# Kernel optimization log

Measured on AMD Instinct MI355X. Metric: run time of the kernel, lower is better.

Reference implementation:

```python
import jax, jax.numpy as jnp
import numpy as np
from jax import lax

B, N_ENT, D_ENT = 64, 512, 256
C_SCAT, C_MAP, W = 32, 18, 64
N_RES = 4


def conv2d(x, w, stride, pad):
    return lax.conv_general_dilated(x, w, (stride, stride), [(pad, pad), (pad, pad)],
                                    dimension_numbers=('NCHW', 'OIHW', 'NCHW'))


def batchnorm(x, g, b, eps=1e-5):
    # training-mode BN (batch statistics), matching nn.BatchNorm2d default train()
    mu = x.mean((0, 2, 3), keepdims=True)
    var = x.var((0, 2, 3), keepdims=True)
    return g[None, :, None, None] * (x - mu) * lax.rsqrt(var + eps) + b[None, :, None, None]


def setup_inputs() -> dict:
    key = jax.random.key(0)
    ks = jax.random.split(key, 24)
    s = 0.05
    inp = {
        'x': jax.random.uniform(ks[0], (B, C_MAP, W, W), jnp.float32),
        'entity_embeddings': jax.random.normal(ks[1], (B, N_ENT, D_ENT), jnp.float32),
        'entity_x_y': jax.random.randint(ks[2], (B, N_ENT, 16), 0, 2, jnp.int32),
        'conv1_w': jax.random.normal(ks[3], (C_SCAT, D_ENT), jnp.float32) * s,
        'project_w': jax.random.normal(ks[4], (32, C_SCAT + C_MAP, 1, 1), jnp.float32) * s,
        'project_b': jnp.zeros((32,), jnp.float32),
        'ds1_w': jax.random.normal(ks[5], (64, 32, 4, 4), jnp.float32) * s,
        'ds1_b': jnp.zeros((64,), jnp.float32),
        'ds2_w': jax.random.normal(ks[6], (128, 64, 4, 4), jnp.float32) * s,
        'ds2_b': jnp.zeros((128,), jnp.float32),
        'ds3_w': jax.random.normal(ks[7], (128, 128, 4, 4), jnp.float32) * s,
        'ds3_b': jnp.zeros((128,), jnp.float32),
        'res_conv1_w': jax.random.normal(ks[8], (N_RES, 128, 128, 3, 3), jnp.float32) * s,
        'res_bn1_g': jnp.ones((N_RES, 128), jnp.float32),
        'res_bn1_b': jnp.zeros((N_RES, 128), jnp.float32),
        'res_conv2_w': jax.random.normal(ks[9], (N_RES, 128, 128, 3, 3), jnp.float32) * s,
        'res_bn2_g': jnp.ones((N_RES, 128), jnp.float32),
        'res_bn2_b': jnp.zeros((N_RES, 128), jnp.float32),
        'fc_w': jax.random.normal(ks[10], (256, 8 * 8 * 128), jnp.float32) * s,
        'fc_b': jnp.zeros((256,), jnp.float32),
    }
    return inp


def _scatter(entity_embeddings, entity_x_y, conv1_w):
    # reduced = relu(Conv1d(256->32, k=1)) on entity dim
    reduced = jax.nn.relu(jnp.einsum('bnd,cd->bnc', entity_embeddings, conv1_w))  # [B,N,32]
    bits = entity_x_y
    pow2 = (2 ** jnp.arange(7, -1, -1)).astype(jnp.int32)
    xv = (bits[..., :8] * pow2).sum(-1) // 4   # [B,N] in 0..63
    yv = (bits[..., 8:] * pow2).sum(-1) // 4
    valid = (bits[..., 0] != -1000000000)
    reduced = reduced * valid[..., None].astype(reduced.dtype)
    b_idx = jnp.arange(entity_embeddings.shape[0], dtype=jnp.int32)[:, None]
    flat = (b_idx * (W * W) + yv * W + xv).reshape(-1)
    scat = jax.ops.segment_sum(reduced.reshape(-1, C_SCAT), flat, num_segments=entity_embeddings.shape[0] * W * W)
    return scat.reshape(-1, W, W, C_SCAT).transpose(0, 3, 1, 2)  # [B,32,W,W]


def reference(x, entity_embeddings, entity_x_y, conv1_w, project_w, project_b,
              ds1_w, ds1_b, ds2_w, ds2_b, ds3_w, ds3_b,
              res_conv1_w, res_bn1_g, res_bn1_b, res_conv2_w, res_bn2_g, res_bn2_b,
              fc_w, fc_b):
    scatter_map = _scatter(entity_embeddings, entity_x_y, conv1_w)
    h = jnp.concatenate([scatter_map, x], axis=1)  # [B,50,64,64]
    h = jax.nn.relu(conv2d(h, project_w, 1, 0) + project_b[None, :, None, None])
    h = jax.nn.relu(conv2d(h, ds1_w, 2, 1) + ds1_b[None, :, None, None])   # [B,64,32,32]
    h = jax.nn.relu(conv2d(h, ds2_w, 2, 1) + ds2_b[None, :, None, None])   # [B,128,16,16]
    h = jax.nn.relu(conv2d(h, ds3_w, 2, 1) + ds3_b[None, :, None, None])   # [B,128,8,8]
    map_skip = h
    for i in range(N_RES):
        identity = h
        o = batchnorm(conv2d(h, res_conv1_w[i], 1, 1), res_bn1_g[i], res_bn1_b[i])
        o = jax.nn.relu(o)
        o = batchnorm(conv2d(o, res_conv2_w[i], 1, 1), res_bn2_g[i], res_bn2_b[i])
        h = jax.nn.relu(o + identity)
        map_skip = map_skip + h
    flat = h.reshape(h.shape[0], -1)
    embedded_spatial = jax.nn.relu(flat @ fc_w.T + fc_b)
    return (map_skip, embedded_spatial)
```

## Files before the change

### kernel.cpp

```cpp
#include <hip/hip_runtime.h>
#include <hip/hip_bf16.h>

typedef __attribute__((ext_vector_type(8))) short bf16x8;
typedef __attribute__((ext_vector_type(4))) short bf16x4;
typedef __attribute__((ext_vector_type(4))) float f32x4;

__device__ __forceinline__ short f2bs(float v) {
  __hip_bfloat16 h = __float2bfloat16(v);
  return *reinterpret_cast<short*>(&h);
}

__global__ __launch_bounds__(256) void k_wall(
    const float* __restrict__ rc1w, const float* __restrict__ rc2w,
    const float* __restrict__ d1w, const float* __restrict__ d2w,
    const float* __restrict__ d3w, const float* __restrict__ fcw,
    const float* __restrict__ c1w, const float* __restrict__ pw,
    short* __restrict__ wTr1, short* __restrict__ wTr2, short* __restrict__ wTds1,
    short* __restrict__ wTds2, short* __restrict__ wTds3, short* __restrict__ wfcbf,
    short* __restrict__ wsc, short* __restrict__ wproj,
    float* __restrict__ scatz, float* __restrict__ statsz) {
  __shared__ float ld[128 * 65];
  const int bx = blockIdx.x;
  const int tid = threadIdx.x;
  if (bx < 4608) {
    const float* src = (bx < 2304) ? rc1w : rc2w;
    short* dst = (bx < 2304) ? wTr1 : wTr2;
    const int i = (bx % 2304) * 256 + tid;
    if (i < 589824) {
      const int layer = i / 147456;
      const int rem = i % 147456;
      const int tap = rem / 16384;
      const int r2 = rem & 16383;
      const int co = r2 >> 7, ci = r2 & 127;
      dst[i] = f2bs(src[(((size_t)layer * 16384 + co * 128 + ci) * 9) + tap]);
    }
  } else if (bx < 6272) {
    int CIN, n, base;
    const float* src;
    short* dst;
    if (bx < 4736) { CIN = 32; n = 32768; base = 4608; src = d1w; dst = wTds1; }
    else if (bx < 5248) { CIN = 64; n = 131072; base = 4736; src = d2w; dst = wTds2; }
    else { CIN = 128; n = 262144; base = 5248; src = d3w; dst = wTds3; }
    const int i = (bx - base) * 256 + tid;
    if (i < n) {
      const int COCI = n / 16;
      const int tap = i / COCI;
      const int rem = i % COCI;
      dst[i] = f2bs(src[(size_t)rem * 16 + tap]);
    }
  } else if (bx < 6528) {
    const int j = bx - 6272;
    const float* sp = fcw + (size_t)j * 8192;
    for (int i = tid; i < 8192; i += 256) {
      const int co = i >> 6, pix = i & 63;
      ld[co * 65 + pix] = sp[i];
    }
    __syncthreads();
    short* dp = wfcbf + (size_t)j * 8192;
    for (int i = tid; i < 8192; i += 256) {
      const int pix = i >> 7, co = i & 127;
      dp[i] = f2bs(ld[co * 65 + pix]);
    }
  } else if (bx < 6560) {
    const int i = (bx - 6528) * 256 + tid;
    if (i < 8192) wsc[i] = f2bs(c1w[i]);
  } else if (bx < 6568) {
    const int i = (bx - 6560) * 256 + tid;
    if (i < 2048) {
      const int co = i >> 6, k = i & 63;
      wproj[i] = (k < 50) ? f2bs(pw[co * 50 + k]) : (short)0;
    }
  } else if (bx < 7080) {
    float4* dst = (float4*)(scatz + (size_t)(bx - 6568) * 16384);
    const float4 z = {0.f, 0.f, 0.f, 0.f};
    for (int t = tid; t < 4096; t += 256) dst[t] = z;
  } else {
    for (int i = tid; i < 2064; i += 256) statsz[i] = 0.f;
  }
}

__global__ __launch_bounds__(256) void k_scatmfma(const float* __restrict__ emb,
                                                  const int* __restrict__ xy,
                                                  const short* __restrict__ wsc,
                                                  float* __restrict__ scat_pm) {
  constexpr int CIP = 264;
  __shared__ short abf[64 * CIP];
  __shared__ int flat[64];
  const int tid = threadIdx.x;
  const int e0 = blockIdx.x * 64;
  const float4* eg = (const float4*)(emb + (size_t)e0 * 256);
  for (int i = tid; i < 4096; i += 256) {
    const int e = i >> 6, k4 = i & 63;
    const float4 v = eg[(size_t)e * 64 + k4];
    bf16x4 o;
    o[0] = f2bs(v.x); o[1] = f2bs(v.y); o[2] = f2bs(v.z); o[3] = f2bs(v.w);
    *(bf16x4*)(&abf[e * CIP + k4 * 4]) = o;
  }
  if (tid < 64) {
    const int* bp = xy + (size_t)(e0 + tid) * 16;
    int xv = 0, yv = 0;
#pragma unroll
    for (int j = 0; j < 8; ++j) xv = (xv << 1) | bp[j];
#pragma unroll
    for (int j = 8; j < 16; ++j) yv = (yv << 1) | bp[j];
    flat[tid] = (bp[0] != -1000000000)
                    ? (((e0 + tid) >> 9) * 4096 + ((yv >> 2) << 6) + (xv >> 2))
                    : -1;
  }
  __syncthreads();
  const int wq = __builtin_amdgcn_readfirstlane(tid >> 6);
  const int lane = tid & 63;
  const int l15 = lane & 15, quad = lane >> 4;
  f32x4 acc[2];
  acc[0] = (f32x4){0.f, 0.f, 0.f, 0.f};
  acc[1] = (f32x4){0.f, 0.f, 0.f, 0.f};
  const short* arow = &abf[(wq * 16 + l15) * CIP + quad * 8];
  const short* w0 = wsc + (size_t)l15 * 256 + quad * 8;
  const short* w1 = wsc + (size_t)(16 + l15) * 256 + quad * 8;
#pragma unroll
  for (int kk = 0; kk < 8; ++kk) {
    bf16x8 a = *(const bf16x8*)(arow + kk * 32);
    acc[0] = __builtin_amdgcn_mfma_f32_16x16x32_bf16(a, *(const bf16x8*)(w0 + kk * 32), acc[0], 0, 0, 0);
    acc[1] = __builtin_amdgcn_mfma_f32_16x16x32_bf16(a, *(const bf16x8*)(w1 + kk * 32), acc[1], 0, 0, 0);
  }
#pragma unroll
  for (int nt = 0; nt < 2; ++nt)
#pragma unroll
    for (int r = 0; r < 4; ++r) {
      const int e = wq * 16 + quad * 4 + r;
      const float v = acc[nt][r];
      const int f = flat[e];
      if (f >= 0 && v > 0.f)
        atomicAdd(&scat_pm[(size_t)f * 32 + nt * 16 + l15], v);
    }
}

__global__ __launch_bounds__(256) void k_projmfma(const float* __restrict__ scat_pm,
                                                  const float* __restrict__ xin,
                                                  const short* __restrict__ wproj,
                                                  const float* __restrict__ pb,
                                                  short* __restrict__ h0pm) {
  constexpr int PK = 72;
  __shared__ short abf[128 * PK];
  const int tid = threadIdx.x;
  const int b = blockIdx.x >> 5;
  const int yx0 = (blockIdx.x & 31) << 7;
  const float4* sg = (const float4*)(scat_pm + ((size_t)(b * 4096 + yx0)) * 32);
  for (int i = tid; i < 1024; i += 256) {
    const int p = i >> 3, c4 = i & 7;
    const float4 v = sg[(size_t)p * 8 + c4];
    bf16x4 o;
    o[0] = f2bs(v.x); o[1] = f2bs(v.y); o[2] = f2bs(v.z); o[3] = f2bs(v.w);
    *(bf16x4*)(&abf[p * PK + c4 * 4]) = o;
  }
  for (int i = tid; i < 2304; i += 256) {
    const int run = i >> 7, p = i & 127;
    abf[p * PK + 32 + run] = f2bs(xin[(size_t)(b * 18 + run) * 4096 + yx0 + p]);
  }
  for (int i = tid; i < 2048; i += 256) {
    const int p = i >> 4, k = 50 + (i & 15);
    abf[p * PK + k] = 0;
  }
  __syncthreads();
  const int wq = __builtin_amdgcn_readfirstlane(tid >> 6);
  const int lane = tid & 63;
  const int l15 = lane & 15, quad = lane >> 4;
  f32x4 acc[2][2];
#pragma unroll
  for (int t = 0; t < 2; ++t)
#pragma unroll
    for (int n = 0; n < 2; ++n) acc[t][n] = (f32x4){0.f, 0.f, 0.f, 0.f};
  const short* wb0 = wproj + (size_t)l15 * 64 + quad * 8;
  const short* wb1 = wproj + (size_t)(16 + l15) * 64 + quad * 8;
#pragma unroll
  for (int kk = 0; kk < 2; ++kk) {
    const bf16x8 b0 = *(const bf16x8*)(wb0 + kk * 32);
    const bf16x8 b1 = *(const bf16x8*)(wb1 + kk * 32);
#pragma unroll
    for (int t = 0; t < 2; ++t) {
      const int pix = (wq * 2 + t) * 16 + l15;
      bf16x8 a = *(const bf16x8*)(&abf[pix * PK + quad * 8 + kk * 32]);
      acc[t][0] = __builtin_amdgcn_mfma_f32_16x16x32_bf16(a, b0, acc[t][0], 0, 0, 0);
      acc[t][1] = __builtin_amdgcn_mfma_f32_16x16x32_bf16(a, b1, acc[t][1], 0, 0, 0);
    }
  }
#pragma unroll
  for (int t = 0; t < 2; ++t)
#pragma unroll
    for (int n = 0; n < 2; ++n) {
      const int co = n * 16 + l15;
      const float bv = pb[co];
#pragma unroll
      for (int r = 0; r < 4; ++r) {
        const int pix = (wq * 2 + t) * 16 + quad * 4 + r;
        float v = acc[t][n][r] + bv;
        v = v > 0.f ? v : 0.f;
        h0pm[((size_t)(b * 4096 + yx0 + pix)) * 32 + co] = f2bs(v);
      }
    }
}

template <int CIN, int COUT, int HIN, int ROWSO, int COSPLIT, int MT, int NT, int OUTMODE>
__global__ __launch_bounds__(256) void k_ds2(const short* __restrict__ inpm,
                                             const short* __restrict__ wT,
                                             const float* __restrict__ bias,
                                             short* __restrict__ outbf,
                                             float* __restrict__ outf,
                                             float* __restrict__ msf) {
  constexpr int HOUT = HIN / 2;
  constexpr int ROWS = 2 * ROWSO + 2;
  constexpr int COLS = HIN + 2;
  constexpr int CHUNKS = CIN / 8;
  constexpr int KK = CIN / 32;
  constexpr int CIPAD = CIN + 8;
  constexpr int NHO = HOUT / ROWSO;
  __shared__ short lin[ROWS * COLS * CIPAD];
  const int tid = threadIdx.x;
  int bx = blockIdx.x;
  const int co_blk = (COSPLIT > 1) ? (bx % COSPLIT) : 0;
  if (COSPLIT > 1) bx /= COSPLIT;
  const int hoblk = bx % NHO;
  const int b = bx / NHO;
  for (int i = tid; i < ROWS * COLS * CHUNKS; i += 256) {
    const int ch = i % CHUNKS;
    const int pixv = i / CHUNKS;
    const int r = pixv / COLS, c = pixv % COLS;
    const int hi = 2 * ROWSO * hoblk - 1 + r;
    const int wc = c - 1;
    bf16x8 v = (bf16x8)(short)0;
    if (hi >= 0 && hi < HIN && wc >= 0 && wc < HIN)
      v = *(const bf16x8*)(inpm + ((size_t)(b * HIN + hi) * HIN + wc) * CIN + ch * 8);
    *(bf16x8*)(&lin[(r * COLS + c) * CIPAD + ch * 8]) = v;
  }
  __syncthreads();
  const int wq = __builtin_amdgcn_readfirstlane(tid >> 6);
  const int lane = tid & 63;
  const int l15 = lane & 15, quad = lane >> 4;
  const int mtile = (MT > 1) ? (wq % MT) : 0;
  const int cogrp = wq / MT;
  const int cobase = co_blk * (COUT / COSPLIT) + cogrp * (NT * 16);
  const int p = mtile * 16 + l15;
  const int dr = p / HOUT;
  const int col = p % HOUT;
  f32x4 acc[NT];
#pragma unroll
  for (int n = 0; n < NT; ++n) acc[n] = (f32x4){0.f, 0.f, 0.f, 0.f};
  const short* wrow = wT + (size_t)(cobase + l15) * CIN + quad * 8;
  for (int ky = 0; ky < 4; ++ky) {
    for (int kx = 0; kx < 4; ++kx) {
      const short* arow = &lin[((2 * dr + ky) * COLS + 2 * col + kx) * CIPAD + quad * 8];
      const short* wt = wrow + (size_t)(ky * 4 + kx) * COUT * CIN;
#pragma unroll
      for (int kk = 0; kk < KK; ++kk) {
        bf16x8 a = *(const bf16x8*)(arow + kk * 32);
#pragma unroll
        for (int n = 0; n < NT; ++n) {
          bf16x8 bf = *(const bf16x8*)(wt + n * 16 * CIN + kk * 32);
          acc[n] = __builtin_amdgcn_mfma_f32_16x16x32_bf16(a, bf, acc[n], 0, 0, 0);
        }
      }
    }
  }
#pragma unroll
  for (int n = 0; n < NT; ++n) {
    const int co = cobase + n * 16 + l15;
    const float bv = bias[co];
#pragma unroll
    for (int r = 0; r < 4; ++r) {
      const int pp = mtile * 16 + quad * 4 + r;
      const int dr2 = pp / HOUT;
      const int c2 = pp % HOUT;
      const int ho = hoblk * ROWSO + dr2;
      float v = acc[n][r] + bv;
      v = v > 0.f ? v : 0.f;
      const size_t o = ((size_t)b * HOUT * HOUT + ho * HOUT + c2) * COUT + co;
      outbf[o] = f2bs(v);
      if (OUTMODE == 1) {
        outf[o] = v;
        msf[o] = v;
      }
    }
  }
}

template <int BNIN>
__global__ __launch_bounds__(256) void k_resmfma(const short* __restrict__ hbfin,
                                                 const float* __restrict__ fin,
                                                 const float* __restrict__ statsIn,
                                                 const float* __restrict__ gIn,
                                                 const float* __restrict__ bIn,
                                                 const short* __restrict__ wT,
                                                 float* __restrict__ outpm,
                                                 float* __restrict__ statsOut) {
  constexpr int CIPAD = 136;
  __shared__ short lin[100 * CIPAD];
  __shared__ float bnsc[128], bnsh[128];
  const int tid = threadIdx.x;
  const int b = blockIdx.x >> 3;
  const int cobase = (blockIdx.x & 7) << 4;
  if (BNIN == 1) {
    if (tid < 128) {
      const float mu = statsIn[tid] * (1.f / 4096.f);
      const float var = statsIn[128 + tid] * (1.f / 4096.f) - mu * mu;
      const float sc = gIn[tid] * rsqrtf(var + 1e-5f);
      bnsc[tid] = sc;
      bnsh[tid] = bIn[tid] - mu * sc;
    }
    __syncthreads();
  }
  if (BNIN == 0) {
    const short* hb = hbfin + ((size_t)b << 13);
    for (int i = tid; i < 1600; i += 256) {
      const int pixel = i >> 4, ch = i & 15;
      const int r = pixel / 10, c = pixel % 10;
      bf16x8 v = (bf16x8)(short)0;
      if (r >= 1 && r <= 8 && c >= 1 && c <= 8)
        v = *(const bf16x8*)(hb + (((r - 1) << 3) + (c - 1)) * 128 + ch * 8);
      *(bf16x8*)(&lin[pixel * CIPAD + ch * 8]) = v;
    }
  } else {
    const float* fb = fin + ((size_t)b << 13);
    for (int i = tid; i < 3200; i += 256) {
      const int pixel = i >> 5, c4 = i & 31;
      const int r = pixel / 10, c = pixel % 10;
      bf16x4 o = (bf16x4)(short)0;
      if (r >= 1 && r <= 8 && c >= 1 && c <= 8) {
        const float4 x = *(const float4*)(fb + (size_t)(((r - 1) << 3) + (c - 1)) * 128 + c4 * 4);
        const float xv[4] = {x.x, x.y, x.z, x.w};
#pragma unroll
        for (int k = 0; k < 4; ++k) {
          const int ci = c4 * 4 + k;
          const float v = xv[k] * bnsc[ci] + bnsh[ci];
          o[k] = f2bs(v > 0.f ? v : 0.f);
        }
      }
      *(bf16x4*)(&lin[pixel * CIPAD + c4 * 4]) = o;
    }
  }
  __syncthreads();
  const int wq = __builtin_amdgcn_readfirstlane(tid >> 6);
  const int lane = tid & 63;
  const int l15 = lane & 15, quad = lane >> 4;
  const int p = wq * 16 + l15;
  const int py = p >> 3, px = p & 7;
  f32x4 acc = (f32x4){0.f, 0.f, 0.f, 0.f};
  const short* wrow = wT + (size_t)(cobase + l15) * 128 + quad * 8;
  for (int t = 0; t < 9; ++t) {
    const int ky = t / 3, kx = t % 3;
    const short* arow = &lin[((py + ky) * 10 + px + kx) * CIPAD + quad * 8];
    const short* wt = wrow + (size_t)t * 16384;
#pragma unroll
    for (int kk = 0; kk < 4; ++kk) {
      bf16x8 a = *(const bf16x8*)(arow + kk * 32);
      bf16x8 bf = *(const bf16x8*)(wt + kk * 32);
      acc = __builtin_amdgcn_mfma_f32_16x16x32_bf16(a, bf, acc, 0, 0, 0);
    }
  }
  float* ob = outpm + ((size_t)b << 13);
  const int co = cobase + l15;
  float s = 0.f, q = 0.f;
#pragma unroll
  for (int r = 0; r < 4; ++r) {
    const float v = acc[r];
    ob[(size_t)(wq * 16 + quad * 4 + r) * 128 + co] = v;
    s += v;
    q += v * v;
  }
  s += __shfl_down(s, 32); q += __shfl_down(q, 32);
  s += __shfl_down(s, 16); q += __shfl_down(q, 16);
  if (lane < 16) {
    atomicAdd(&statsOut[co], s);
    atomicAdd(&statsOut[128 + co], q);
  }
}

__global__ __launch_bounds__(256) void k_resA(const float* __restrict__ tmp2,
                                              const float* __restrict__ statsB,
                                              const float* __restrict__ g2,
                                              const float* __restrict__ b2,
                                              const float* __restrict__ identf,
                                              float* __restrict__ houtf,
                                              float* __restrict__ mspm,
                                              const short* __restrict__ wT,
                                              float* __restrict__ outpm,
                                              float* __restrict__ statsOut) {
  constexpr int CIPAD = 136;
  __shared__ short lin[100 * CIPAD];
  __shared__ float bnsc[128], bnsh[128];
  const int tid = threadIdx.x;
  const int b = blockIdx.x >> 3;
  const int cobase = (blockIdx.x & 7) << 4;
  if (tid < 128) {
    const float mu = statsB[tid] * (1.f / 4096.f);
    const float var = statsB[128 + tid] * (1.f / 4096.f) - mu * mu;
    const float sc = g2[tid] * rsqrtf(var + 1e-5f);
    bnsc[tid] = sc;
    bnsh[tid] = b2[tid] - mu * sc;
  }
  __syncthreads();
  const float* fb = tmp2 + ((size_t)b << 13);
  const float* idb = identf + ((size_t)b << 13);
  for (int t = tid; t < 3200; t += 256) {
    const int pixel = t >> 5, c4 = t & 31;
    const int r = pixel / 10, c = pixel % 10;
    bf16x4 o = (bf16x4)(short)0;
    if (r >= 1 && r <= 8 && c >= 1 && c <= 8) {
      const size_t p8 = (size_t)(((r - 1) << 3) + (c - 1)) * 128 + c4 * 4;
      const float4 x = *(const float4*)(fb + p8);
      const float4 id = *(const float4*)(idb + p8);
      const float xv[4] = {x.x, x.y, x.z, x.w};
      const float iv[4] = {id.x, id.y, id.z, id.w};
#pragma unroll
      for (int k = 0; k < 4; ++k) {
        const int ci = c4 * 4 + k;
        const float v = xv[k] * bnsc[ci] + bnsh[ci] + iv[k];
        o[k] = f2bs(v > 0.f ? v : 0.f);
      }
    }
    *(bf16x4*)(&lin[pixel * CIPAD + c4 * 4]) = o;
  }
  for (int t = tid; t < 1024; t += 256) {
    const int pix = t >> 4, cl = t & 15;
    const int cow = cobase + cl;
    const size_t o = ((size_t)b << 13) + (size_t)pix * 128 + cow;
    float v = tmp2[o] * bnsc[cow] + bnsh[cow] + identf[o];
    v = v > 0.f ? v : 0.f;
    houtf[o] = v;
    mspm[o] += v;
  }
  __syncthreads();
  const int wq = __builtin_amdgcn_readfirstlane(tid >> 6);
  const int lane = tid & 63;
  const int l15 = lane & 15, quad = lane >> 4;
  const int p = wq * 16 + l15;
  const int py = p >> 3, px = p & 7;
  f32x4 acc = (f32x4){0.f, 0.f, 0.f, 0.f};
  const short* wrow = wT + (size_t)(cobase + l15) * 128 + quad * 8;
  for (int t = 0; t < 9; ++t) {
    const int ky = t / 3, kx = t % 3;
    const short* arow = &lin[((py + ky) * 10 + px + kx) * CIPAD + quad * 8];
    const short* wt = wrow + (size_t)t * 16384;
#pragma unroll
    for (int kk = 0; kk < 4; ++kk) {
      bf16x8 a = *(const bf16x8*)(arow + kk * 32);
      bf16x8 bf = *(const bf16x8*)(wt + kk * 32);
      acc = __builtin_amdgcn_mfma_f32_16x16x32_bf16(a, bf, acc, 0, 0, 0);
    }
  }
  float* ob = outpm + ((size_t)b << 13);
  const int co = cobase + l15;
  float s = 0.f, q = 0.f;
#pragma unroll
  for (int r = 0; r < 4; ++r) {
    const float v = acc[r];
    ob[(size_t)(wq * 16 + quad * 4 + r) * 128 + co] = v;
    s += v;
    q += v * v;
  }
  s += __shfl_down(s, 32); q += __shfl_down(q, 32);
  s += __shfl_down(s, 16); q += __shfl_down(q, 16);
  if (lane < 16) {
    atomicAdd(&statsOut[co], s);
    atomicAdd(&statsOut[128 + co], q);
  }
}

__global__ __launch_bounds__(256) void k_msfin(const float* __restrict__ tmp2,
                                               const float* __restrict__ statsB,
                                               const float* __restrict__ g2,
                                               const float* __restrict__ b2,
                                               const float* __restrict__ identf,
                                               const float* __restrict__ mspm,
                                               short* __restrict__ hbf,
                                               float* __restrict__ out0) {
  __shared__ float t[64 * 132];
  __shared__ float bnsc[128], bnsh[128];
  const int b = blockIdx.x;
  const int tid = threadIdx.x;
  if (tid < 128) {
    const float mu = statsB[tid] * (1.f / 4096.f);
    const float var = statsB[128 + tid] * (1.f / 4096.f) - mu * mu;
    const float sc = g2[tid] * rsqrtf(var + 1e-5f);
    bnsc[tid] = sc;
    bnsh[tid] = b2[tid] - mu * sc;
  }
  __syncthreads();
  const size_t base = (size_t)b << 13;
  for (int i = tid; i < 8192; i += 256) {
    const int pix = i >> 7, co = i & 127;
    float v = tmp2[base + i] * bnsc[co] + bnsh[co] + identf[base + i];
    v = v > 0.f ? v : 0.f;
    hbf[base + i] = f2bs(v);
    t[pix * 132 + co] = mspm[base + i] + v;
  }
  __syncthreads();
  for (int i = tid; i < 8192; i += 256) {
    const int co = i >> 6, pix = i & 63;
    out0[base + i] = t[pix * 132 + co];
  }
}

__global__ __launch_bounds__(256) void k_fcmfma(const short* __restrict__ hbf,
                                                const short* __restrict__ wbf,
                                                float* __restrict__ part) {
  const int nb = blockIdx.x & 3;
  const int kb = blockIdx.x >> 2;
  const int wq = __builtin_amdgcn_readfirstlane((int)(threadIdx.x >> 6));
  const int lane = threadIdx.x & 63;
  const int l15 = lane & 15, quad = lane >> 4;
  const int k0 = kb * 256 + quad * 8;
  const short* wp = wbf + (size_t)(nb * 64 + wq * 16 + l15) * 8192 + k0;
  const short* hp = hbf + (size_t)l15 * 8192 + k0;
  f32x4 acc[4];
#pragma unroll
  for (int m = 0; m < 4; ++m) acc[m] = (f32x4){0.f, 0.f, 0.f, 0.f};
  for (int ks = 0; ks < 8; ++ks) {
    bf16x8 bfr = *(const bf16x8*)(wp + ks * 32);
#pragma unroll
    for (int m = 0; m < 4; ++m) {
      bf16x8 a = *(const bf16x8*)(hp + (size_t)m * 16 * 8192 + ks * 32);
      acc[m] = __builtin_amdgcn_mfma_f32_16x16x32_bf16(a, bfr, acc[m], 0, 0, 0);
    }
  }
#pragma unroll
  for (int m = 0; m < 4; ++m)
#pragma unroll
    for (int r = 0; r < 4; ++r) {
      const int b = m * 16 + quad * 4 + r;
      part[((size_t)kb * 64 + b) * 256 + nb * 64 + wq * 16 + l15] = acc[m][r];
    }
}

__global__ __launch_bounds__(256) void k_fcred(const float* __restrict__ part,
                                               const float* __restrict__ bias,
                                               float* __restrict__ out1) {
  const int idx = blockIdx.x * 256 + threadIdx.x;
  const int j = idx & 255;
  float s = 0.f;
#pragma unroll 8
  for (int kb = 0; kb < 32; ++kb) s += part[(size_t)kb * 16384 + idx];
  const float v = s + bias[j];
  out1[idx] = v > 0.f ? v : 0.f;
}

extern "C" void kernel_launch(void* const* d_in, const int* in_sizes, int n_in,
                              void* d_out, int out_size, void* d_ws, size_t ws_size,
                              hipStream_t stream) {
  const float* xin = (const float*)d_in[0];
  const float* emb = (const float*)d_in[1];
  const int* xy = (const int*)d_in[2];
  const float* c1w = (const float*)d_in[3];
  const float* pw = (const float*)d_in[4];
  const float* pb = (const float*)d_in[5];
  const float* d1w = (const float*)d_in[6];
  const float* d1b = (const float*)d_in[7];
  const float* d2w = (const float*)d_in[8];
  const float* d2b = (const float*)d_in[9];
  const float* d3w = (const float*)d_in[10];
  const float* d3b = (const float*)d_in[11];
  const float* rc1w = (const float*)d_in[12];
  const float* rbn1g = (const float*)d_in[13];
  const float* rbn1b = (const float*)d_in[14];
  const float* rc2w = (const float*)d_in[15];
  const float* rbn2g = (const float*)d_in[16];
  const float* rbn2b = (const float*)d_in[17];
  const float* fcw = (const float*)d_in[18];
  const float* fcb = (const float*)d_in[19];

  float* out0 = (float*)d_out;
  float* out1 = out0 + 524288;

  float* F = (float*)d_ws;
  float* scat = F + 0;
  short* h1pm = (short*)(F + 0);
  short* h2pm = (short*)(F + 2097152);
  float* hApm = F + 3145728;
  float* hBpm = F + 3670016;
  float* tmppm = F + 4194304;
  float* tmp2pm = F + 4718592;
  float* mspm = F + 5242880;
  short* pmbfA = (short*)(F + 5767168);
  short* hbf = (short*)(F + 6029312);
  float* stats = F + 6291456;
  float* fcpart = F + 6293504;
  short* h0pm = (short*)(F + 8388608);
  short* wfcbf = (short*)(F + 12582912);
  short* wTr1 = (short*)(F + 13631488);
  short* wTr2 = wTr1 + 589824;
  short* wTds1 = wTr2 + 589824;
  short* wTds2 = wTds1 + 32768;
  short* wTds3 = wTds2 + 131072;
  short* wsc = wTds3 + 262144;
  short* wproj = wsc + 8192;

  k_wall<<<7081, 256, 0, stream>>>(rc1w, rc2w, d1w, d2w, d3w, fcw, c1w, pw,
                                   wTr1, wTr2, wTds1, wTds2, wTds3, wfcbf, wsc, wproj,
                                   scat, stats);
  k_scatmfma<<<512, 256, 0, stream>>>(emb, xy, wsc, scat);
  k_projmfma<<<2048, 256, 0, stream>>>(scat, xin, wproj, pb, h0pm);
  k_ds2<32, 64, 64, 2, 1, 4, 4, 0><<<1024, 256, 0, stream>>>(h0pm, wTds1, d1b, h1pm, nullptr, nullptr);
  k_ds2<64, 128, 32, 1, 1, 1, 2, 0><<<1024, 256, 0, stream>>>(h1pm, wTds2, d2b, h2pm, nullptr, nullptr);
  k_ds2<128, 128, 16, 2, 2, 1, 1, 1><<<512, 256, 0, stream>>>(h2pm, wTds3, d3b, pmbfA, hApm, mspm);

  k_resmfma<0><<<512, 256, 0, stream>>>(pmbfA, nullptr, nullptr, nullptr, nullptr,
                                        wTr1, tmppm, stats);
  k_resmfma<1><<<512, 256, 0, stream>>>(nullptr, tmppm, stats, rbn1g, rbn1b,
                                        wTr2, tmp2pm, stats + 256);
  float* idp = hApm;
  float* hop = hBpm;
  for (int i = 1; i < 4; ++i) {
    k_resA<<<512, 256, 0, stream>>>(tmp2pm, stats + (i - 1) * 512 + 256,
                                    rbn2g + (i - 1) * 128, rbn2b + (i - 1) * 128,
                                    idp, hop, mspm, wTr1 + (size_t)i * 147456,
                                    tmppm, stats + i * 512);
    k_resmfma<1><<<512, 256, 0, stream>>>(nullptr, tmppm, stats + i * 512,
                                          rbn1g + i * 128, rbn1b + i * 128,
                                          wTr2 + (size_t)i * 147456, tmp2pm,
                                          stats + i * 512 + 256);
    float* sw = idp; idp = hop; hop = sw;
  }
  k_msfin<<<64, 256, 0, stream>>>(tmp2pm, stats + 3 * 512 + 256, rbn2g + 3 * 128,
                                  rbn2b + 3 * 128, idp, mspm, hbf, out0);
  k_fcmfma<<<128, 256, 0, stream>>>(hbf, wfcbf, fcpart);
  k_fcred<<<64, 256, 0, stream>>>(fcpart, fcb, out1);
}
```

Before: 404.4 us.

## Widen residual conv blocks to 32 channels and fuse FC into one kernel

Residual conv kernels now compute 32 output channels per block with two MFMA accumulators sharing each A fragment. This halves the grid and the redundant LDS staging of the padded input tile per batch. The split-K FC plus its reduction kernel is replaced by a single 16-block kernel that runs the full K loop with bias and ReLU fused, removing the partial-sum buffer and one launch. The risk is lower parallelism: 256 blocks for the convs and only 16 blocks each looping over 8192 K for the FC.

```diff
diff --git a/kernel.cpp b/kernel.cpp
--- a/kernel.cpp
+++ b/kernel.cpp
@@ -296,8 +296,8 @@
   __shared__ short lin[100 * CIPAD];
   __shared__ float bnsc[128], bnsh[128];
   const int tid = threadIdx.x;
-  const int b = blockIdx.x >> 3;
-  const int cobase = (blockIdx.x & 7) << 4;
+  const int b = blockIdx.x >> 2;
+  const int cobase = (blockIdx.x & 3) << 5;
   if (BNIN == 1) {
     if (tid < 128) {
       const float mu = statsIn[tid] * (1.f / 4096.f);
@@ -343,34 +343,42 @@
   const int l15 = lane & 15, quad = lane >> 4;
   const int p = wq * 16 + l15;
   const int py = p >> 3, px = p & 7;
-  f32x4 acc = (f32x4){0.f, 0.f, 0.f, 0.f};
-  const short* wrow = wT + (size_t)(cobase + l15) * 128 + quad * 8;
+  f32x4 acc[2];
+  acc[0] = (f32x4){0.f, 0.f, 0.f, 0.f};
+  acc[1] = (f32x4){0.f, 0.f, 0.f, 0.f};
+  const short* wrow0 = wT + (size_t)(cobase + l15) * 128 + quad * 8;
+  const short* wrow1 = wrow0 + 16 * 128;
   for (int t = 0; t < 9; ++t) {
     const int ky = t / 3, kx = t % 3;
     const short* arow = &lin[((py + ky) * 10 + px + kx) * CIPAD + quad * 8];
-    const short* wt = wrow + (size_t)t * 16384;
+    const size_t toff = (size_t)t * 16384;
 #pragma unroll
     for (int kk = 0; kk < 4; ++kk) {
       bf16x8 a = *(const bf16x8*)(arow + kk * 32);
-      bf16x8 bf = *(const bf16x8*)(wt + kk * 32);
-      acc = __builtin_amdgcn_mfma_f32_16x16x32_bf16(a, bf, acc, 0, 0, 0);
+      acc[0] = __builtin_amdgcn_mfma_f32_16x16x32_bf16(a, *(const bf16x8*)(wrow0 + toff + kk * 32), acc[0], 0, 0, 0);
+      acc[1] = __builtin_amdgcn_mfma_f32_16x16x32_bf16(a, *(const bf16x8*)(wrow1 + toff + kk * 32), acc[1], 0, 0, 0);
     }
   }
   float* ob = outpm + ((size_t)b << 13);
-  const int co = cobase + l15;
-  float s = 0.f, q = 0.f;
-#pragma unroll
-  for (int r = 0; r < 4; ++r) {
-    const float v = acc[r];
-    ob[(size_t)(wq * 16 + quad * 4 + r) * 128 + co] = v;
-    s += v;
-    q += v * v;
-  }
-  s += __shfl_down(s, 32); q += __shfl_down(q, 32);
-  s += __shfl_down(s, 16); q += __shfl_down(q, 16);
+  float s[2] = {0.f, 0.f}, q[2] = {0.f, 0.f};
+#pragma unroll
+  for (int n = 0; n < 2; ++n) {
+    const int co = cobase + n * 16 + l15;
+#pragma unroll
+    for (int r = 0; r < 4; ++r) {
+      const float v = acc[n][r];
+      ob[(size_t)(wq * 16 + quad * 4 + r) * 128 + co] = v;
+      s[n] += v;
+      q[n] += v * v;
+    }
+    s[n] += __shfl_down(s[n], 32); q[n] += __shfl_down(q[n], 32);
+    s[n] += __shfl_down(s[n], 16); q[n] += __shfl_down(q[n], 16);
+  }
   if (lane < 16) {
-    atomicAdd(&statsOut[co], s);
-    atomicAdd(&statsOut[128 + co], q);
+    atomicAdd(&statsOut[cobase + lane], s[0]);
+    atomicAdd(&statsOut[128 + cobase + lane], q[0]);
+    atomicAdd(&statsOut[cobase + 16 + lane], s[1]);
+    atomicAdd(&statsOut[128 + cobase + 16 + lane], q[1]);
   }
 }
 
@@ -388,8 +396,8 @@
   __shared__ short lin[100 * CIPAD];
   __shared__ float bnsc[128], bnsh[128];
   const int tid = threadIdx.x;
-  const int b = blockIdx.x >> 3;
-  const int cobase = (blockIdx.x & 7) << 4;
+  const int b = blockIdx.x >> 2;
+  const int cobase = (blockIdx.x & 3) << 5;
   if (tid < 128) {
     const float mu = statsB[tid] * (1.f / 4096.f);
     const float var = statsB[128 + tid] * (1.f / 4096.f) - mu * mu;
@@ -419,8 +427,8 @@
     }
     *(bf16x4*)(&lin[pixel * CIPAD + c4 * 4]) = o;
   }
-  for (int t = tid; t < 1024; t += 256) {
-    const int pix = t >> 4, cl = t & 15;
+  for (int t = tid; t < 2048; t += 256) {
+    const int pix = t >> 5, cl = t & 31;
     const int cow = cobase + cl;
     const size_t o = ((size_t)b << 13) + (size_t)pix * 128 + cow;
     float v = tmp2[o] * bnsc[cow] + bnsh[cow] + identf[o];
@@ -434,34 +442,42 @@
   const int l15 = lane & 15, quad = lane >> 4;
   const int p = wq * 16 + l15;
   const int py = p >> 3, px = p & 7;
-  f32x4 acc = (f32x4){0.f, 0.f, 0.f, 0.f};
-  const short* wrow = wT + (size_t)(cobase + l15) * 128 + quad * 8;
+  f32x4 acc[2];
+  acc[0] = (f32x4){0.f, 0.f, 0.f, 0.f};
+  acc[1] = (f32x4){0.f, 0.f, 0.f, 0.f};
+  const short* wrow0 = wT + (size_t)(cobase + l15) * 128 + quad * 8;
+  const short* wrow1 = wrow0 + 16 * 128;
   for (int t = 0; t < 9; ++t) {
     const int ky = t / 3, kx = t % 3;
     const short* arow = &lin[((py + ky) * 10 + px + kx) * CIPAD + quad * 8];
-    const short* wt = wrow + (size_t)t * 16384;
+    const size_t toff = (size_t)t * 16384;
 #pragma unroll
     for (int kk = 0; kk < 4; ++kk) {
       bf16x8 a = *(const bf16x8*)(arow + kk * 32);
-      bf16x8 bf = *(const bf16x8*)(wt + kk * 32);
-      acc = __builtin_amdgcn_mfma_f32_16x16x32_bf16(a, bf, acc, 0, 0, 0);
+      acc[0] = __builtin_amdgcn_mfma_f32_16x16x32_bf16(a, *(const bf16x8*)(wrow0 + toff + kk * 32), acc[0], 0, 0, 0);
+      acc[1] = __builtin_amdgcn_mfma_f32_16x16x32_bf16(a, *(const bf16x8*)(wrow1 + toff + kk * 32), acc[1], 0, 0, 0);
     }
   }
   float* ob = outpm + ((size_t)b << 13);
-  const int co = cobase + l15;
-  float s = 0.f, q = 0.f;
-#pragma unroll
-  for (int r = 0; r < 4; ++r) {
-    const float v = acc[r];
-    ob[(size_t)(wq * 16 + quad * 4 + r) * 128 + co] = v;
-    s += v;
-    q += v * v;
-  }
-  s += __shfl_down(s, 32); q += __shfl_down(q, 32);
-  s += __shfl_down(s, 16); q += __shfl_down(q, 16);
+  float s[2] = {0.f, 0.f}, q[2] = {0.f, 0.f};
+#pragma unroll
+  for (int n = 0; n < 2; ++n) {
+    const int co = cobase + n * 16 + l15;
+#pragma unroll
+    for (int r = 0; r < 4; ++r) {
+      const float v = acc[n][r];
+      ob[(size_t)(wq * 16 + quad * 4 + r) * 128 + co] = v;
+      s[n] += v;
+      q[n] += v * v;
+    }
+    s[n] += __shfl_down(s[n], 32); q[n] += __shfl_down(q[n], 32);
+    s[n] += __shfl_down(s[n], 16); q[n] += __shfl_down(q[n], 16);
+  }
   if (lane < 16) {
-    atomicAdd(&statsOut[co], s);
-    atomicAdd(&statsOut[128 + co], q);
+    atomicAdd(&statsOut[cobase + lane], s[0]);
+    atomicAdd(&statsOut[128 + cobase + lane], q[0]);
+    atomicAdd(&statsOut[cobase + 16 + lane], s[1]);
+    atomicAdd(&statsOut[128 + cobase + 16 + lane], q[1]);
   }
 }
 
@@ -500,47 +516,38 @@
   }
 }
 
-__global__ __launch_bounds__(256) void k_fcmfma(const short* __restrict__ hbf,
-                                                const short* __restrict__ wbf,
-                                                float* __restrict__ part) {
-  const int nb = blockIdx.x & 3;
-  const int kb = blockIdx.x >> 2;
+__global__ __launch_bounds__(256) void k_fc1(const short* __restrict__ hbf,
+                                             const short* __restrict__ wbf,
+                                             const float* __restrict__ bias,
+                                             float* __restrict__ out1) {
+  const int jb = blockIdx.x & 3;
+  const int mb = blockIdx.x >> 2;
   const int wq = __builtin_amdgcn_readfirstlane((int)(threadIdx.x >> 6));
   const int lane = threadIdx.x & 63;
   const int l15 = lane & 15, quad = lane >> 4;
-  const int k0 = kb * 256 + quad * 8;
-  const short* wp = wbf + (size_t)(nb * 64 + wq * 16 + l15) * 8192 + k0;
-  const short* hp = hbf + (size_t)l15 * 8192 + k0;
+  const short* hp = hbf + (size_t)(mb * 16 + l15) * 8192 + quad * 8;
+  const short* wp = wbf + (size_t)(jb * 64 + wq * 16 + l15) * 8192 + quad * 8;
   f32x4 acc[4];
 #pragma unroll
-  for (int m = 0; m < 4; ++m) acc[m] = (f32x4){0.f, 0.f, 0.f, 0.f};
-  for (int ks = 0; ks < 8; ++ks) {
-    bf16x8 bfr = *(const bf16x8*)(wp + ks * 32);
-#pragma unroll
-    for (int m = 0; m < 4; ++m) {
-      bf16x8 a = *(const bf16x8*)(hp + (size_t)m * 16 * 8192 + ks * 32);
-      acc[m] = __builtin_amdgcn_mfma_f32_16x16x32_bf16(a, bfr, acc[m], 0, 0, 0);
-    }
-  }
-#pragma unroll
-  for (int m = 0; m < 4; ++m)
-#pragma unroll
-    for (int r = 0; r < 4; ++r) {
-      const int b = m * 16 + quad * 4 + r;
-      part[((size_t)kb * 64 + b) * 256 + nb * 64 + wq * 16 + l15] = acc[m][r];
-    }
-}
-
-__global__ __launch_bounds__(256) void k_fcred(const float* __restrict__ part,
-                                               const float* __restrict__ bias,
-                                               float* __restrict__ out1) {
-  const int idx = blockIdx.x * 256 + threadIdx.x;
-  const int j = idx & 255;
-  float s = 0.f;
-#pragma unroll 8
-  for (int kb = 0; kb < 32; ++kb) s += part[(size_t)kb * 16384 + idx];
-  const float v = s + bias[j];
-  out1[idx] = v > 0.f ? v : 0.f;
+  for (int u = 0; u < 4; ++u) acc[u] = (f32x4){0.f, 0.f, 0.f, 0.f};
+  for (int k = 0; k < 8192; k += 128) {
+#pragma unroll
+    for (int u = 0; u < 4; ++u)
+      acc[u] = __builtin_amdgcn_mfma_f32_16x16x32_bf16(*(const bf16x8*)(hp + k + u * 32),
+                                                       *(const bf16x8*)(wp + k + u * 32),
+                                                       acc[u], 0, 0, 0);
+  }
+  f32x4 sum;
+#pragma unroll
+  for (int r = 0; r < 4; ++r) sum[r] = (acc[0][r] + acc[1][r]) + (acc[2][r] + acc[3][r]);
+  const int j = jb * 64 + wq * 16 + l15;
+  const float bv = bias[j];
+#pragma unroll
+  for (int r = 0; r < 4; ++r) {
+    const int m = mb * 16 + quad * 4 + r;
+    const float v = sum[r] + bv;
+    out1[(size_t)m * 256 + j] = v > 0.f ? v : 0.f;
+  }
 }
 
 extern "C" void kernel_launch(void* const* d_in, const int* in_sizes, int n_in,
@@ -582,7 +589,6 @@
   short* pmbfA = (short*)(F + 5767168);
   short* hbf = (short*)(F + 6029312);
   float* stats = F + 6291456;
-  float* fcpart = F + 6293504;
   short* h0pm = (short*)(F + 8388608);
   short* wfcbf = (short*)(F + 12582912);
   short* wTr1 = (short*)(F + 13631488);
@@ -602,18 +608,18 @@
   k_ds2<64, 128, 32, 1, 1, 1, 2, 0><<<1024, 256, 0, stream>>>(h1pm, wTds2, d2b, h2pm, nullptr, nullptr);
   k_ds2<128, 128, 16, 2, 2, 1, 1, 1><<<512, 256, 0, stream>>>(h2pm, wTds3, d3b, pmbfA, hApm, mspm);
 
-  k_resmfma<0><<<512, 256, 0, stream>>>(pmbfA, nullptr, nullptr, nullptr, nullptr,
+  k_resmfma<0><<<256, 256, 0, stream>>>(pmbfA, nullptr, nullptr, nullptr, nullptr,
                                         wTr1, tmppm, stats);
-  k_resmfma<1><<<512, 256, 0, stream>>>(nullptr, tmppm, stats, rbn1g, rbn1b,
+  k_resmfma<1><<<256, 256, 0, stream>>>(nullptr, tmppm, stats, rbn1g, rbn1b,
                                         wTr2, tmp2pm, stats + 256);
   float* idp = hApm;
   float* hop = hBpm;
   for (int i = 1; i < 4; ++i) {
-    k_resA<<<512, 256, 0, stream>>>(tmp2pm, stats + (i - 1) * 512 + 256,
+    k_resA<<<256, 256, 0, stream>>>(tmp2pm, stats + (i - 1) * 512 + 256,
                                     rbn2g + (i - 1) * 128, rbn2b + (i - 1) * 128,
                                     idp, hop, mspm, wTr1 + (size_t)i * 147456,
                                     tmppm, stats + i * 512);
-    k_resmfma<1><<<512, 256, 0, stream>>>(nullptr, tmppm, stats + i * 512,
+    k_resmfma<1><<<256, 256, 0, stream>>>(nullptr, tmppm, stats + i * 512,
                                           rbn1g + i * 128, rbn1b + i * 128,
                                           wTr2 + (size_t)i * 147456, tmp2pm,
                                           stats + i * 512 + 256);
@@ -621,6 +627,5 @@
   }
   k_msfin<<<64, 256, 0, stream>>>(tmp2pm, stats + 3 * 512 + 256, rbn2g + 3 * 128,
                                   rbn2b + 3 * 128, idp, mspm, hbf, out0);
-  k_fcmfma<<<128, 256, 0, stream>>>(hbf, wfcbf, fcpart);
-  k_fcred<<<64, 256, 0, stream>>>(fcpart, fcb, out1);
-}
+  k_fc1<<<16, 256, 0, stream>>>(hbf, wfcbf, fcb, out1);
+}
```

New measurement: 470.6 us. 1.16x slower.
